# Kernel optimization log

Hardware: AMD Instinct MI355X
Metric: run time of the kernel (lower is better)

## Reference

```python
import jax, jax.numpy as jnp
import numpy as np

B, S, H, NH = 2, 2048, 768, 12
HD = H // NH  # 64
MAXPOS = 2048


def _rope_tables(max_pos, d):
    # bert4torch get_sinusoid_encoding_table: even cols sin, odd cols cos
    pos = np.arange(max_pos, dtype=np.float32)[:, None]
    div = np.exp(np.arange(0, d, 2, dtype=np.float32) * (-np.log(10000.0) / d))
    tab = np.zeros((max_pos, d), np.float32)
    tab[:, 0::2] = np.sin(pos * div)
    tab[:, 1::2] = np.cos(pos * div)
    cos = np.concatenate([tab[:, 1::2], tab[:, 1::2]], axis=1)  # [:,1::2].repeat(1,2)
    sin = np.concatenate([tab[:, 0::2], tab[:, 0::2]], axis=1)  # [:,0::2].repeat(1,2)
    return jnp.asarray(cos), jnp.asarray(sin)


def setup_inputs() -> dict:
    key = jax.random.key(0)
    ks = jax.random.split(key, 10)
    s = 0.02
    inp = {}
    inp["hidden_states"] = jax.random.normal(ks[0], (B, S, H), jnp.float32)
    inp["attention_mask"] = jnp.ones((B, 1, 1, S), jnp.float32)
    for i, n in enumerate(["q", "k", "v", "o"]):
        inp[f"W{n}"] = (jax.random.normal(ks[1 + i], (H, H), jnp.float32) * s)
        inp[f"b{n}"] = jnp.zeros((H,), jnp.float32)
    cos, sin = _rope_tables(MAXPOS, HD)
    inp["cos_position"] = cos
    inp["sin_position"] = sin
    return inp


def _apply_rope(qw, cos, sin):
    # Faithful to source: seq_len_dim defaults to 1, which on a
    # [B, heads, S, head_dim] tensor is the HEADS axis.
    L = qw.shape[1]
    qw2 = jnp.concatenate([-qw[..., 1::2], qw[..., 0::2]], axis=-1)
    return qw * cos[:L][None, :, None, :] + qw2 * sin[:L][None, :, None, :]


def reference(hidden_states, attention_mask, Wq, bq, Wk, bk, Wv, bv, Wo, bo,
              cos_position, sin_position):
    b, s, _ = hidden_states.shape

    def heads(x):  # [b,s,H] -> [b,NH,s,HD]
        return x.reshape(b, s, NH, HD).transpose(0, 2, 1, 3)

    q = heads(hidden_states @ Wq + bq)
    k = heads(hidden_states @ Wk + bk)
    v = heads(hidden_states @ Wv + bv)
    q = _apply_rope(q, cos_position, sin_position)
    k = _apply_rope(k, cos_position, sin_position)
    scores = jnp.einsum('bnid,bnjd->bnij', q, k) / jnp.sqrt(jnp.float32(HD))
    scores = scores + (1.0 - attention_mask) * (-10000.0)
    probs = jax.nn.softmax(scores, axis=-1)  # dropout is identity in eval
    ctx = jnp.einsum('bnij,bnjd->bnid', probs, v)
    ctx = ctx.transpose(0, 2, 1, 3).reshape(b, s, H)
    return ctx @ Wo + bo
```

## Files before the change

### kernel.cpp

```cpp
#include <hip/hip_runtime.h>

#define B 2
#define S 2048
#define H 768
#define NH 12
#define HD 64
#define BS (B * S)
#define LOG2E 1.4426950408889634f

typedef unsigned short u16;
typedef short short8 __attribute__((ext_vector_type(8)));
typedef float f32x4 __attribute__((ext_vector_type(4)));
typedef float f32x16 __attribute__((ext_vector_type(16)));

__device__ __forceinline__ u16 f2bf(float f) {
    union { float f; unsigned u; } c; c.f = f;
    unsigned u = c.u + 0x7FFFu + ((c.u >> 16) & 1u);
    return (u16)(u >> 16);
}
__device__ __forceinline__ float bf2f(u16 h) {
    union { unsigned u; float f; } c; c.u = ((unsigned)h) << 16;
    return c.f;
}
__device__ __forceinline__ f32x16 zero16() {
    f32x16 v;
    #pragma unroll
    for (int i = 0; i < 16; ++i) v[i] = 0.f;
    return v;
}

__device__ __forceinline__ void g2l16(const u16* g, u16* l) {
    __builtin_amdgcn_global_load_lds(
        (const __attribute__((address_space(1))) void*)g,
        (__attribute__((address_space(3))) void*)l, 16, 0, 0);
}

__global__ __launch_bounds__(256) void prep_hs_kernel(
    const float* __restrict__ src, u16* __restrict__ dst)
{
    size_t i = ((size_t)blockIdx.x * 256 + threadIdx.x) * 8;
    float4 a = *(const float4*)(src + i);
    float4 b = *(const float4*)(src + i + 4);
    short8 p;
    p[0] = (short)f2bf(a.x); p[1] = (short)f2bf(a.y);
    p[2] = (short)f2bf(a.z); p[3] = (short)f2bf(a.w);
    p[4] = (short)f2bf(b.x); p[5] = (short)f2bf(b.y);
    p[6] = (short)f2bf(b.z); p[7] = (short)f2bf(b.w);
    *(short8*)(dst + i) = p;
}

__global__ __launch_bounds__(256) void prep_w_kernel(
    const float* __restrict__ Wq, const float* __restrict__ Wk,
    const float* __restrict__ Wv, const float* __restrict__ Wo,
    const float* __restrict__ bq, const float* __restrict__ bk,
    const float* __restrict__ cosp, const float* __restrict__ sinp,
    u16* __restrict__ WTqkv, u16* __restrict__ WTo,
    float* __restrict__ bqk2)
{
    __shared__ float Lt[64 * 65];
    const int t = threadIdx.x;
    const int z = blockIdx.z;
    const float* W = (z == 0) ? Wq : (z == 1) ? Wk : (z == 2) ? Wv : Wo;
    u16* D = (z == 3) ? WTo : (WTqkv + (size_t)z * H * H);
    const int k0 = blockIdx.x * 64, n0 = blockIdx.y * 64;
    const int head = n0 >> 6;
    const float scl = (z == 0) ? (0.125f * LOG2E) : 1.0f;

    if (z < 2 && blockIdx.x == 0 && t < 64) {
        const float* bs = (z == 0) ? bq : bk;
        int d = t;
        int pd = (d < 32) ? (2 * d + 1) : (2 * (d - 32));
        float sv = ((d < 32) ? -1.f : 1.f) * sinp[head * HD + d];
        float cv = cosp[head * HD + d];
        bqk2[z * H + n0 + d] = scl * (cv * bs[n0 + d] + sv * bs[n0 + pd]);
    }

    #pragma unroll
    for (int u = 0; u < 4; ++u) {
        int f = t + u * 256;
        int r = f >> 4, c4 = (f & 15) * 4;
        float4 w = *(const float4*)(W + (size_t)(k0 + r) * H + n0 + c4);
        Lt[r * 65 + c4 + 0] = w.x; Lt[r * 65 + c4 + 1] = w.y;
        Lt[r * 65 + c4 + 2] = w.z; Lt[r * 65 + c4 + 3] = w.w;
    }
    __syncthreads();
    #pragma unroll
    for (int u = 0; u < 4; ++u) {
        int f = t + u * 256;
        int n = f >> 4, k4 = (f & 15) * 4;
        ushort4 p;
        if (z < 2) {
            int pn = (n < 32) ? (2 * n + 1) : (2 * (n - 32));
            float cv = scl * cosp[head * HD + n];
            float sv = scl * ((n < 32) ? -1.f : 1.f) * sinp[head * HD + n];
            p.x = f2bf(cv * Lt[(k4 + 0) * 65 + n] + sv * Lt[(k4 + 0) * 65 + pn]);
            p.y = f2bf(cv * Lt[(k4 + 1) * 65 + n] + sv * Lt[(k4 + 1) * 65 + pn]);
            p.z = f2bf(cv * Lt[(k4 + 2) * 65 + n] + sv * Lt[(k4 + 2) * 65 + pn]);
            p.w = f2bf(cv * Lt[(k4 + 3) * 65 + n] + sv * Lt[(k4 + 3) * 65 + pn]);
        } else {
            p.x = f2bf(Lt[(k4 + 0) * 65 + n]);
            p.y = f2bf(Lt[(k4 + 1) * 65 + n]);
            p.z = f2bf(Lt[(k4 + 2) * 65 + n]);
            p.w = f2bf(Lt[(k4 + 3) * 65 + n]);
        }
        *(ushort4*)(D + (size_t)(n0 + n) * H + k0 + k4) = p;
    }
}

__global__ __launch_bounds__(256) void gemm_qkv_kernel(
    const u16* __restrict__ A, const u16* __restrict__ BT,
    const float* __restrict__ bqk2, const float* __restrict__ bv,
    u16* __restrict__ Qb, u16* __restrict__ Kb, u16* __restrict__ VT)
{
    __shared__ alignas(16) u16 As[128 * 64];
    __shared__ alignas(16) u16 Bs[128 * 64];

    const int tid  = threadIdx.x;
    const int w    = tid >> 6;
    const int lane = tid & 63;
    const int quad = lane >> 4;
    const int l15  = lane & 15;
    const int wm = (w & 1) * 64, wn = (w >> 1) * 64;
    const int m0 = blockIdx.x * 128;
    const int n0 = blockIdx.y * 128;

    int srow[4], slc[4];
    #pragma unroll
    for (int u = 0; u < 4; ++u) {
        int s = u * 256 + tid;
        srow[u] = s >> 3;
        slc[u]  = (s & 7) ^ (srow[u] & 7);
    }

    f32x4 acc[4][4];
    #pragma unroll
    for (int i = 0; i < 4; ++i)
        #pragma unroll
        for (int j = 0; j < 4; ++j) acc[i][j] = (f32x4){0.f, 0.f, 0.f, 0.f};

    for (int k0 = 0; k0 < H; k0 += 64) {
        __syncthreads();
        #pragma unroll
        for (int u = 0; u < 4; ++u) {
            g2l16(A  + (size_t)(m0 + srow[u]) * H + k0 + slc[u] * 8,
                  As + (u * 256 + w * 64) * 8);
            g2l16(BT + (size_t)(n0 + srow[u]) * H + k0 + slc[u] * 8,
                  Bs + (u * 256 + w * 64) * 8);
        }
        __syncthreads();
        #pragma unroll
        for (int kc = 0; kc < 2; ++kc) {
            const int ch = kc * 4 + quad;
            short8 af[4], bf[4];
            #pragma unroll
            for (int mi = 0; mi < 4; ++mi) {
                int row = wm + mi * 16 + l15;
                af[mi] = *(const short8*)&As[row * 64 + (ch ^ (row & 7)) * 8];
            }
            #pragma unroll
            for (int ni = 0; ni < 4; ++ni) {
                int row = wn + ni * 16 + l15;
                bf[ni] = *(const short8*)&Bs[row * 64 + (ch ^ (row & 7)) * 8];
            }
            #pragma unroll
            for (int mi = 0; mi < 4; ++mi)
                #pragma unroll
                for (int ni = 0; ni < 4; ++ni)
                    acc[mi][ni] = __builtin_amdgcn_mfma_f32_16x16x32_bf16(
                        af[mi], bf[ni], acc[mi][ni], 0, 0, 0);
        }
    }

    #pragma unroll
    for (int mi = 0; mi < 4; ++mi) {
        const int mbase = m0 + wm + mi * 16 + quad * 4;
        #pragma unroll
        for (int ni = 0; ni < 4; ++ni) {
            const int col = n0 + wn + ni * 16 + l15;
            const int which = col / H;
            const int c = col - which * H;
            const int h = c >> 6, d = c & 63;
            if (which == 2) {
                const float bias = bv[c];
                const int b_ = mbase >> 11, s = mbase & (S - 1);
                ushort4 pk;
                pk.x = f2bf(acc[mi][ni][0] + bias);
                pk.y = f2bf(acc[mi][ni][1] + bias);
                pk.z = f2bf(acc[mi][ni][2] + bias);
                pk.w = f2bf(acc[mi][ni][3] + bias);
                *(ushort4*)&VT[(((size_t)b_ * NH + h) * HD + d) * S + s] = pk;
            } else {
                u16* dst = (which == 0) ? Qb : Kb;
                const float bias = bqk2[which * H + c];
                #pragma unroll
                for (int r = 0; r < 4; ++r) {
                    int m = mbase + r;
                    int b_ = m >> 11, s = m & (S - 1);
                    dst[(((size_t)b_ * NH + h) * S + s) * HD + d] =
                        f2bf(acc[mi][ni][r] + bias);
                }
            }
        }
    }
}

__global__ __launch_bounds__(256) void gemm_out_kernel(
    const u16* __restrict__ A, const u16* __restrict__ BT,
    const float* __restrict__ bo, float* __restrict__ out)
{
    __shared__ alignas(16) u16 As[128 * 72];
    __shared__ alignas(16) u16 Bs[64 * 72];

    const int tid  = threadIdx.x;
    const int w    = tid >> 6;
    const int lane = tid & 63;
    const int quad = lane >> 4;
    const int l15  = lane & 15;
    const int wm = (w & 1) * 64, wn = (w >> 1) * 32;
    const int m0 = blockIdx.x * 128;
    const int n0 = blockIdx.y * 64;
    const int lr = tid >> 3, lc8 = (tid & 7) * 8;

    f32x4 acc[4][2];
    #pragma unroll
    for (int i = 0; i < 4; ++i)
        #pragma unroll
        for (int j = 0; j < 2; ++j) acc[i][j] = (f32x4){0.f, 0.f, 0.f, 0.f};

    short8 pa[2], pa2[2], pb[2];
    #pragma unroll
    for (int u = 0; u < 2; ++u) {
        pa[u]  = *(const short8*)(A  + (size_t)(m0 + lr + u * 32) * H + lc8);
        pa2[u] = *(const short8*)(A  + (size_t)(m0 + lr + 64 + u * 32) * H + lc8);
        pb[u]  = *(const short8*)(BT + (size_t)(n0 + lr + u * 32) * H + lc8);
    }

    for (int k0 = 0; k0 < H; k0 += 64) {
        __syncthreads();
        #pragma unroll
        for (int u = 0; u < 2; ++u) {
            *(short8*)&As[(lr + u * 32) * 72 + lc8] = pa[u];
            *(short8*)&As[(lr + 64 + u * 32) * 72 + lc8] = pa2[u];
            *(short8*)&Bs[(lr + u * 32) * 72 + lc8] = pb[u];
        }
        if (k0 + 64 < H) {
            #pragma unroll
            for (int u = 0; u < 2; ++u) {
                pa[u]  = *(const short8*)(A  + (size_t)(m0 + lr + u * 32) * H + k0 + 64 + lc8);
                pa2[u] = *(const short8*)(A  + (size_t)(m0 + lr + 64 + u * 32) * H + k0 + 64 + lc8);
                pb[u]  = *(const short8*)(BT + (size_t)(n0 + lr + u * 32) * H + k0 + 64 + lc8);
            }
        }
        __syncthreads();
        #pragma unroll
        for (int kc = 0; kc < 64; kc += 32) {
            short8 af[4], bf[2];
            #pragma unroll
            for (int mi = 0; mi < 4; ++mi)
                af[mi] = *(const short8*)&As[(wm + mi * 16 + l15) * 72 + kc + quad * 8];
            #pragma unroll
            for (int ni = 0; ni < 2; ++ni)
                bf[ni] = *(const short8*)&Bs[(wn + ni * 16 + l15) * 72 + kc + quad * 8];
            #pragma unroll
            for (int mi = 0; mi < 4; ++mi)
                #pragma unroll
                for (int ni = 0; ni < 2; ++ni)
                    acc[mi][ni] = __builtin_amdgcn_mfma_f32_16x16x32_bf16(
                        af[mi], bf[ni], acc[mi][ni], 0, 0, 0);
        }
    }

    #pragma unroll
    for (int mi = 0; mi < 4; ++mi) {
        const int mbase = m0 + wm + mi * 16 + quad * 4;
        #pragma unroll
        for (int ni = 0; ni < 2; ++ni) {
            const int col = n0 + wn + ni * 16 + l15;
            const float bias = bo[col];
            #pragma unroll
            for (int r = 0; r < 4; ++r)
                out[(size_t)(mbase + r) * H + col] = acc[mi][ni][r] + bias;
        }
    }
}

__global__ __launch_bounds__(256) void attn_mfma_kernel(
    const u16* __restrict__ Q, const u16* __restrict__ K,
    const u16* __restrict__ VT, const float* __restrict__ mask,
    u16* __restrict__ ctx)
{
    __shared__ alignas(16) u16 smem[21504];
    u16* const Kbase = smem;
    u16* const Vbase = smem + 8192;
    u16* const Psw   = smem + 16384 + (threadIdx.x >> 6) * 1280;

    const int tid  = threadIdx.x;
    const int w    = tid >> 6;
    const int lane = tid & 63;
    const int l31  = lane & 31;
    const int h5   = lane >> 5;
    const int rh   = w & 1;
    const int kh   = w >> 1;
    const int bn = blockIdx.y, b = bn / NH, hh = bn % NH;
    const int q0 = blockIdx.x * 64;
    const int NT = S / 64;

    short8 qa[4];
    {
        const u16* Qp = Q + ((size_t)bn * S + q0 + rh * 32 + l31) * HD + h5 * 8;
        #pragma unroll
        for (int kc = 0; kc < 4; ++kc)
            qa[kc] = *(const short8*)(Qp + kc * 16);
    }

    const u16* Kg = K + (size_t)bn * S * HD;
    const u16* Vg = VT + (size_t)bn * HD * S;
    const float* mrow = mask + (size_t)b * S;

    int srow[2], slc[2];
    #pragma unroll
    for (int u = 0; u < 2; ++u) {
        int s = u * 256 + tid;
        srow[u] = s >> 3;
        slc[u]  = (s & 7) ^ (srow[u] & 7);
    }

    #define STAGE(JT, NB)                                                     \
        _Pragma("unroll")                                                     \
        for (int u = 0; u < 2; ++u) {                                         \
            g2l16(Kg + (size_t)((JT) * 64 + srow[u]) * HD + slc[u] * 8,       \
                  Kbase + (NB) * 4096 + (u * 256 + w * 64) * 8);              \
            g2l16(Vg + (size_t)srow[u] * S + (JT) * 64 + slc[u] * 8,          \
                  Vbase + (NB) * 4096 + (u * 256 + w * 64) * 8);              \
        }

    STAGE(0, 0)

    f32x16 o0 = zero16(), o1 = zero16();
    float l_p[16];
    #pragma unroll
    for (int i = 0; i < 16; ++i) l_p[i] = 0.f;

    for (int jt = 0; jt < NT; ++jt) {
        const int cur = jt & 1;
        const float mv = mrow[jt * 64 + kh * 32 + l31];
        __syncthreads();
        if (jt + 1 < NT) { STAGE(jt + 1, cur ^ 1) }

        const u16* Kc = Kbase + cur * 4096;
        const u16* Vc = Vbase + cur * 4096;

        f32x16 sc = zero16();
        {
            const int krow = kh * 32 + l31;
            const int sw = krow & 7;
            #pragma unroll
            for (int kc = 0; kc < 4; ++kc) {
                const short8 kb =
                    *(const short8*)&Kc[krow * 64 + ((kc * 2 + h5) ^ sw) * 8];
                sc = __builtin_amdgcn_mfma_f32_32x32x16_bf16(qa[kc], kb, sc, 0, 0, 0);
            }
        }

        const float mt = (1.0f - mv) * (-10000.0f * LOG2E);
        #pragma unroll
        for (int reg = 0; reg < 16; ++reg) {
            float p = __builtin_amdgcn_exp2f(sc[reg] + mt);
            l_p[reg] += p;
            const int r32 = (reg & 3) + 8 * (reg >> 2) + 4 * h5;
            Psw[r32 * 40 + l31] = f2bf(p);
        }

        asm volatile("s_waitcnt lgkmcnt(0)" ::: "memory");

        const short8 pa0 = *(const short8*)&Psw[l31 * 40 + h5 * 8];
        const short8 pa1 = *(const short8*)&Psw[l31 * 40 + 16 + h5 * 8];

        #pragma unroll
        for (int nt = 0; nt < 2; ++nt) {
            const int vrow = nt * 32 + l31;
            const int sw = vrow & 7;
            const short8 vb0 =
                *(const short8*)&Vc[vrow * 64 + ((kh * 4 + h5) ^ sw) * 8];
            const short8 vb1 =
                *(const short8*)&Vc[vrow * 64 + ((kh * 4 + 2 + h5) ^ sw) * 8];
            f32x16& o = nt ? o1 : o0;
            o = __builtin_amdgcn_mfma_f32_32x32x16_bf16(pa0, vb0, o, 0, 0, 0);
            o = __builtin_amdgcn_mfma_f32_32x32x16_bf16(pa1, vb1, o, 0, 0, 0);
        }
    }
    #undef STAGE

    #pragma unroll
    for (int reg = 0; reg < 16; ++reg) {
        #pragma unroll
        for (int off = 16; off >= 1; off >>= 1)
            l_p[reg] += __shfl_xor(l_p[reg], off, 32);
    }

    __syncthreads();
    float* cb = (float*)smem;
    float* lb = (float*)(smem + 16384);

    if (kh == 1) {
        float* c = cb + rh * 2048;
        #pragma unroll
        for (int reg = 0; reg < 16; ++reg) {
            float2 v = make_float2(o0[reg], o1[reg]);
            *(float2*)&c[reg * 128 + lane * 2] = v;
        }
        if (l31 == 0) {
            #pragma unroll
            for (int reg = 0; reg < 16; ++reg)
                lb[rh * 32 + h5 * 16 + reg] = l_p[reg];
        }
    }
    __syncthreads();
    if (kh == 0) {
        const float* c = cb + rh * 2048;
        #pragma unroll
        for (int reg = 0; reg < 16; ++reg) {
            float2 po = *(const float2*)&c[reg * 128 + lane * 2];
            float lt = l_p[reg] + lb[rh * 32 + h5 * 16 + reg];
            float inv = 1.0f / lt;
            const int r32 = (reg & 3) + 8 * (reg >> 2) + 4 * h5;
            const int s = q0 + rh * 32 + r32;
            u16* dst = ctx + ((size_t)b * S + s) * H + hh * 64;
            dst[l31]      = f2bf((o0[reg] + po.x) * inv);
            dst[32 + l31] = f2bf((o1[reg] + po.y) * inv);
        }
    }
}

extern "C" void kernel_launch(void* const* d_in, const int* in_sizes, int n_in,
                              void* d_out, int out_size, void* d_ws, size_t ws_size,
                              hipStream_t stream)
{
    const float* hs   = (const float*)d_in[0];
    const float* mask = (const float*)d_in[1];
    const float* Wq   = (const float*)d_in[2];
    const float* bq   = (const float*)d_in[3];
    const float* Wk   = (const float*)d_in[4];
    const float* bk   = (const float*)d_in[5];
    const float* Wv   = (const float*)d_in[6];
    const float* bv   = (const float*)d_in[7];
    const float* Wo   = (const float*)d_in[8];
    const float* bo   = (const float*)d_in[9];
    const float* cosp = (const float*)d_in[10];
    const float* sinp = (const float*)d_in[11];
    float* out = (float*)d_out;

    const size_t per = (size_t)B * NH * S * HD;
    u16* ws    = (u16*)d_ws;
    u16* hsb   = ws;
    u16* WTqkv = hsb + per;
    u16* WTo   = WTqkv + (size_t)3 * H * H;
    u16* Qb    = WTo + (size_t)H * H;
    u16* Kb    = Qb + per;
    u16* VT    = Kb + per;
    u16* ctxb  = VT + per;
    float* bqk2 = (float*)(ctxb + per);

    prep_hs_kernel<<<(BS * H) / 2048, 256, 0, stream>>>(hs, hsb);
    prep_w_kernel<<<dim3(12, 12, 4), 256, 0, stream>>>(
        Wq, Wk, Wv, Wo, bq, bk, cosp, sinp, WTqkv, WTo, bqk2);

    gemm_qkv_kernel<<<dim3(BS / 128, 2304 / 128), 256, 0, stream>>>(
        hsb, WTqkv, bqk2, bv, Qb, Kb, VT);

    attn_mfma_kernel<<<dim3(S / 64, B * NH), 256, 0, stream>>>(
        Qb, Kb, VT, mask, ctxb);

    gemm_out_kernel<<<dim3(BS / 128, H / 64), 256, 0, stream>>>(
        ctxb, WTo, bo, out);
}
```

Measured before the change: 195.8 us.

## Double-buffer GEMM LDS tiles with async loads and merge prep kernels

The QKV and output projection GEMMs now keep two LDS buffers per operand. The next K-slice is issued with global_load_lds while MFMAs run on the current slice, which removes one barrier per iteration. The output GEMM also moves from register-staged copies into padded LDS to direct async loads with an XOR-swizzled layout. The two preprocessing kernels become one launch to save launch overhead. In exchange, LDS use doubles, which may lower occupancy, and correctness depends on the barrier waiting for the async loads to finish.

Result: faster. 191.3 us (-2.3%).

```diff
diff --git a/kernel.cpp b/kernel.cpp
--- a/kernel.cpp
+++ b/kernel.cpp
@@ -35,38 +35,41 @@
         (__attribute__((address_space(3))) void*)l, 16, 0, 0);
 }
 
-__global__ __launch_bounds__(256) void prep_hs_kernel(
-    const float* __restrict__ src, u16* __restrict__ dst)
-{
-    size_t i = ((size_t)blockIdx.x * 256 + threadIdx.x) * 8;
-    float4 a = *(const float4*)(src + i);
-    float4 b = *(const float4*)(src + i + 4);
-    short8 p;
-    p[0] = (short)f2bf(a.x); p[1] = (short)f2bf(a.y);
-    p[2] = (short)f2bf(a.z); p[3] = (short)f2bf(a.w);
-    p[4] = (short)f2bf(b.x); p[5] = (short)f2bf(b.y);
-    p[6] = (short)f2bf(b.z); p[7] = (short)f2bf(b.w);
-    *(short8*)(dst + i) = p;
-}
-
-__global__ __launch_bounds__(256) void prep_w_kernel(
+__global__ __launch_bounds__(256) void prep_kernel(
+    const float* __restrict__ hs,
     const float* __restrict__ Wq, const float* __restrict__ Wk,
     const float* __restrict__ Wv, const float* __restrict__ Wo,
     const float* __restrict__ bq, const float* __restrict__ bk,
     const float* __restrict__ cosp, const float* __restrict__ sinp,
-    u16* __restrict__ WTqkv, u16* __restrict__ WTo,
+    u16* __restrict__ hsb, u16* __restrict__ WTqkv, u16* __restrict__ WTo,
     float* __restrict__ bqk2)
 {
     __shared__ float Lt[64 * 65];
+    const int bid = blockIdx.x;
     const int t = threadIdx.x;
-    const int z = blockIdx.z;
+
+    if (bid >= 576) {
+        size_t i = ((size_t)(bid - 576) * 256 + t) * 8;
+        float4 a = *(const float4*)(hs + i);
+        float4 b = *(const float4*)(hs + i + 4);
+        short8 p;
+        p[0] = (short)f2bf(a.x); p[1] = (short)f2bf(a.y);
+        p[2] = (short)f2bf(a.z); p[3] = (short)f2bf(a.w);
+        p[4] = (short)f2bf(b.x); p[5] = (short)f2bf(b.y);
+        p[6] = (short)f2bf(b.z); p[7] = (short)f2bf(b.w);
+        *(short8*)(hsb + i) = p;
+        return;
+    }
+
+    const int z   = bid / 144;
+    const int rem = bid - z * 144;
+    const int k0 = (rem / 12) * 64, n0 = (rem % 12) * 64;
     const float* W = (z == 0) ? Wq : (z == 1) ? Wk : (z == 2) ? Wv : Wo;
     u16* D = (z == 3) ? WTo : (WTqkv + (size_t)z * H * H);
-    const int k0 = blockIdx.x * 64, n0 = blockIdx.y * 64;
     const int head = n0 >> 6;
     const float scl = (z == 0) ? (0.125f * LOG2E) : 1.0f;
 
-    if (z < 2 && blockIdx.x == 0 && t < 64) {
+    if (z < 2 && rem / 12 == 0 && t < 64) {
         const float* bs = (z == 0) ? bq : bk;
         int d = t;
         int pd = (d < 32) ? (2 * d + 1) : (2 * (d - 32));
@@ -112,8 +115,8 @@
     const float* __restrict__ bqk2, const float* __restrict__ bv,
     u16* __restrict__ Qb, u16* __restrict__ Kb, u16* __restrict__ VT)
 {
-    __shared__ alignas(16) u16 As[128 * 64];
-    __shared__ alignas(16) u16 Bs[128 * 64];
+    __shared__ alignas(16) u16 Abuf[2][128 * 64];
+    __shared__ alignas(16) u16 Bbuf[2][128 * 64];
 
     const int tid  = threadIdx.x;
     const int w    = tid >> 6;
@@ -123,6 +126,7 @@
     const int wm = (w & 1) * 64, wn = (w >> 1) * 64;
     const int m0 = blockIdx.x * 128;
     const int n0 = blockIdx.y * 128;
+    const int NK = H / 64;
 
     int srow[4], slc[4];
     #pragma unroll
@@ -132,22 +136,30 @@
         slc[u]  = (s & 7) ^ (srow[u] & 7);
     }
 
+    #define QSTAGE(IT, NB)                                                    \
+        _Pragma("unroll")                                                     \
+        for (int u = 0; u < 4; ++u) {                                         \
+            g2l16(A  + (size_t)(m0 + srow[u]) * H + (IT) * 64 + slc[u] * 8,   \
+                  &Abuf[NB][(u * 256 + w * 64) * 8]);                         \
+            g2l16(BT + (size_t)(n0 + srow[u]) * H + (IT) * 64 + slc[u] * 8,   \
+                  &Bbuf[NB][(u * 256 + w * 64) * 8]);                         \
+        }
+
+    QSTAGE(0, 0)
+
     f32x4 acc[4][4];
     #pragma unroll
     for (int i = 0; i < 4; ++i)
         #pragma unroll
         for (int j = 0; j < 4; ++j) acc[i][j] = (f32x4){0.f, 0.f, 0.f, 0.f};
 
-    for (int k0 = 0; k0 < H; k0 += 64) {
+    for (int it = 0; it < NK; ++it) {
+        const int cur = it & 1;
         __syncthreads();
-        #pragma unroll
-        for (int u = 0; u < 4; ++u) {
-            g2l16(A  + (size_t)(m0 + srow[u]) * H + k0 + slc[u] * 8,
-                  As + (u * 256 + w * 64) * 8);
-            g2l16(BT + (size_t)(n0 + srow[u]) * H + k0 + slc[u] * 8,
-                  Bs + (u * 256 + w * 64) * 8);
-        }
-        __syncthreads();
+        if (it + 1 < NK) { QSTAGE(it + 1, cur ^ 1) }
+
+        const u16* Ac = Abuf[cur];
+        const u16* Bc = Bbuf[cur];
         #pragma unroll
         for (int kc = 0; kc < 2; ++kc) {
             const int ch = kc * 4 + quad;
@@ -155,12 +167,12 @@
             #pragma unroll
             for (int mi = 0; mi < 4; ++mi) {
                 int row = wm + mi * 16 + l15;
-                af[mi] = *(const short8*)&As[row * 64 + (ch ^ (row & 7)) * 8];
+                af[mi] = *(const short8*)&Ac[row * 64 + (ch ^ (row & 7)) * 8];
             }
             #pragma unroll
             for (int ni = 0; ni < 4; ++ni) {
                 int row = wn + ni * 16 + l15;
-                bf[ni] = *(const short8*)&Bs[row * 64 + (ch ^ (row & 7)) * 8];
+                bf[ni] = *(const short8*)&Bc[row * 64 + (ch ^ (row & 7)) * 8];
             }
             #pragma unroll
             for (int mi = 0; mi < 4; ++mi)
@@ -170,6 +182,7 @@
                         af[mi], bf[ni], acc[mi][ni], 0, 0, 0);
         }
     }
+    #undef QSTAGE
 
     #pragma unroll
     for (int mi = 0; mi < 4; ++mi) {
@@ -208,8 +221,8 @@
     const u16* __restrict__ A, const u16* __restrict__ BT,
     const float* __restrict__ bo, float* __restrict__ out)
 {
-    __shared__ alignas(16) u16 As[128 * 72];
-    __shared__ alignas(16) u16 Bs[64 * 72];
+    __shared__ alignas(16) u16 Abuf[2][128 * 64];
+    __shared__ alignas(16) u16 Bbuf[2][64 * 64];
 
     const int tid  = threadIdx.x;
     const int w    = tid >> 6;
@@ -219,7 +232,27 @@
     const int wm = (w & 1) * 64, wn = (w >> 1) * 32;
     const int m0 = blockIdx.x * 128;
     const int n0 = blockIdx.y * 64;
-    const int lr = tid >> 3, lc8 = (tid & 7) * 8;
+    const int NK = H / 64;
+
+    int srow[4], slc[4];
+    #pragma unroll
+    for (int u = 0; u < 4; ++u) {
+        int s = u * 256 + tid;
+        srow[u] = s >> 3;
+        slc[u]  = (s & 7) ^ (srow[u] & 7);
+    }
+
+    #define OSTAGE(IT, NB)                                                    \
+        _Pragma("unroll")                                                     \
+        for (int u = 0; u < 4; ++u)                                           \
+            g2l16(A + (size_t)(m0 + srow[u]) * H + (IT) * 64 + slc[u] * 8,    \
+                  &Abuf[NB][(u * 256 + w * 64) * 8]);                         \
+        _Pragma("unroll")                                                     \
+        for (int u = 0; u < 2; ++u)                                           \
+            g2l16(BT + (size_t)(n0 + srow[u]) * H + (IT) * 64 + slc[u] * 8,   \
+                  &Bbuf[NB][(u * 256 + w * 64) * 8]);
+
+    OSTAGE(0, 0)
 
     f32x4 acc[4][2];
     #pragma unroll
@@ -227,40 +260,27 @@
         #pragma unroll
         for (int j = 0; j < 2; ++j) acc[i][j] = (f32x4){0.f, 0.f, 0.f, 0.f};
 
-    short8 pa[2], pa2[2], pb[2];
-    #pragma unroll
-    for (int u = 0; u < 2; ++u) {
-        pa[u]  = *(const short8*)(A  + (size_t)(m0 + lr + u * 32) * H + lc8);
-        pa2[u] = *(const short8*)(A  + (size_t)(m0 + lr + 64 + u * 32) * H + lc8);
-        pb[u]  = *(const short8*)(BT + (size_t)(n0 + lr + u * 32) * H + lc8);
-    }
-
-    for (int k0 = 0; k0 < H; k0 += 64) {
+    for (int it = 0; it < NK; ++it) {
+        const int cur = it & 1;
         __syncthreads();
-        #pragma unroll
-        for (int u = 0; u < 2; ++u) {
-            *(short8*)&As[(lr + u * 32) * 72 + lc8] = pa[u];
-            *(short8*)&As[(lr + 64 + u * 32) * 72 + lc8] = pa2[u];
-            *(short8*)&Bs[(lr + u * 32) * 72 + lc8] = pb[u];
-        }
-        if (k0 + 64 < H) {
-            #pragma unroll
-            for (int u = 0; u < 2; ++u) {
-                pa[u]  = *(const short8*)(A  + (size_t)(m0 + lr + u * 32) * H + k0 + 64 + lc8);
-                pa2[u] = *(const short8*)(A  + (size_t)(m0 + lr + 64 + u * 32) * H + k0 + 64 + lc8);
-                pb[u]  = *(const short8*)(BT + (size_t)(n0 + lr + u * 32) * H + k0 + 64 + lc8);
-            }
-        }
-        __syncthreads();
-        #pragma unroll
-        for (int kc = 0; kc < 64; kc += 32) {
+        if (it + 1 < NK) { OSTAGE(it + 1, cur ^ 1) }
+
+        const u16* Ac = Abuf[cur];
+        const u16* Bc = Bbuf[cur];
+        #pragma unroll
+        for (int kc = 0; kc < 2; ++kc) {
+            const int ch = kc * 4 + quad;
             short8 af[4], bf[2];
             #pragma unroll
-            for (int mi = 0; mi < 4; ++mi)
-                af[mi] = *(const short8*)&As[(wm + mi * 16 + l15) * 72 + kc + quad * 8];
-            #pragma unroll
-            for (int ni = 0; ni < 2; ++ni)
-                bf[ni] = *(const short8*)&Bs[(wn + ni * 16 + l15) * 72 + kc + quad * 8];
+            for (int mi = 0; mi < 4; ++mi) {
+                int row = wm + mi * 16 + l15;
+                af[mi] = *(const short8*)&Ac[row * 64 + (ch ^ (row & 7)) * 8];
+            }
+            #pragma unroll
+            for (int ni = 0; ni < 2; ++ni) {
+                int row = wn + ni * 16 + l15;
+                bf[ni] = *(const short8*)&Bc[row * 64 + (ch ^ (row & 7)) * 8];
+            }
             #pragma unroll
             for (int mi = 0; mi < 4; ++mi)
                 #pragma unroll
@@ -269,6 +289,7 @@
                         af[mi], bf[ni], acc[mi][ni], 0, 0, 0);
         }
     }
+    #undef OSTAGE
 
     #pragma unroll
     for (int mi = 0; mi < 4; ++mi) {
@@ -461,9 +482,8 @@
     u16* ctxb  = VT + per;
     float* bqk2 = (float*)(ctxb + per);
 
-    prep_hs_kernel<<<(BS * H) / 2048, 256, 0, stream>>>(hs, hsb);
-    prep_w_kernel<<<dim3(12, 12, 4), 256, 0, stream>>>(
-        Wq, Wk, Wv, Wo, bq, bk, cosp, sinp, WTqkv, WTo, bqk2);
+    prep_kernel<<<576 + (BS * H) / 2048, 256, 0, stream>>>(
+        hs, Wq, Wk, Wv, Wo, bq, bk, cosp, sinp, hsb, WTqkv, WTo, bqk2);
 
     gemm_qkv_kernel<<<dim3(BS / 128, 2304 / 128), 256, 0, stream>>>(
         hsb, WTqkv, bqk2, bv, Qb, Kb, VT);
```
